# Performance work log

Measured on AMD Instinct MI355X. Metric: run time of the kernel, lower is better.

## Reference

```python
import jax, jax.numpy as jnp
import numpy as np

jax.config.update("jax_enable_x64", True)

NUM_OF_LSB_TO_IGNORE = 5
COMPARISON_NUM_BITS_IGNORED = 5
SCALE = 65536.0  # activations live on an integer-share-like scale so bit shifts matter

BLOCK_SIZES = np.array([[0, 1]] * 32 + [[2, 2]] * 48 + [[4, 4]] * 48)
# active (non-identity) block sizes and the channel indices they own
ACTIVE = [(tuple(int(v) for v in bs), np.where(np.all(BLOCK_SIZES == bs, axis=1))[0])
          for bs in np.unique(BLOCK_SIZES, axis=0) if 0 not in bs]


def setup_inputs() -> dict:
    key = jax.random.key(0)
    activation = jax.random.normal(key, (16, 128, 114, 114), dtype=jnp.float32) * SCALE
    return {"activation": activation}


def _block_sign(x, bh, bw):
    # x: [N, c, H, W]. Pad bottom/right to block multiples, space-to-depth,
    # integer floor-mean per block, LSB truncation via int16 wrap, sign >= 0.
    N, c, H, W = x.shape
    ph, pw = (-H) % bh, (-W) % bw
    xp = jnp.pad(x, ((0, 0), (0, 0), (0, ph), (0, pw)))
    xr = xp.reshape(N, c, (H + ph) // bh, bh, (W + pw) // bw, bw)
    s = xr.sum(axis=(3, 5)).astype(jnp.int64)          # block sums
    mean = s // (bh * bw)                               # integer floor mean
    q = ((mean >> NUM_OF_LSB_TO_IGNORE).astype(jnp.int16)
         .astype(jnp.int64)) << COMPARISON_NUM_BITS_IGNORED
    sign = q >= 0                                       # DReLU
    # broadcast block sign back to pixels, then unpad
    sign = jnp.repeat(jnp.repeat(sign, bh, axis=2), bw, axis=3)
    return sign[:, :, :H, :W]


def reference(activation):
    out = activation
    for (bh, bw), ch in ACTIVE:  # small fixed set of block-size groups
        cur = activation[:, ch]
        sign = _block_sign(cur, bh, bw)
        out = out.at[:, ch].set(cur * sign.astype(activation.dtype))
    return out
```

## Files before the change

### kernel.cpp

```cpp
#include <hip/hip_runtime.h>


typedef float v4 __attribute__((ext_vector_type(4)));

#define PLANE  12996
#define NBLK_A 6498
#define NU_B   43776
#define NBLK_B 10944
#define NU_C   22272
#define NBLK_C 5568

__global__ __launch_bounds__(256) void sbrelu_reg(const float* __restrict__ in,
                                                  float* __restrict__ out) {
    const int bid = blockIdx.x;
    const int tid = threadIdx.x;

    if (bid < NBLK_A) {
        int idx = bid * 256 + tid;
        int n = idx / 103968;
        int off = n * 415872 + (idx - n * 103968);
        ((v4*)out)[off] = ((const v4*)in)[off];
        return;
    }

    const int lane = tid & 63;
    const int wid  = tid >> 6;

    if (bid < NBLK_A + NBLK_B) {
        int u  = (bid - NBLK_A) * 4 + wid;
        int p  = u / 57;
        int rp = u - 57 * p;
        int n  = p / 48;
        int c  = 32 + (p - 48 * n);
        size_t base = (size_t)(n * 128 + c) * PLANE + 228 * rp;
        if (lane < 57) {
            const float2* i0 = (const float2*)(in + base) + lane;
            float2 a = i0[0];
            float2 b = i0[57];
            float s = ((a.x + a.y) + b.x) + b.y;
            float m = (s > -1.0f) ? 1.0f : 0.0f;
            float2* o0 = (float2*)(out + base) + lane;
            o0[0]  = make_float2(a.x * m, a.y * m);
            o0[57] = make_float2(b.x * m, b.y * m);
        }
        return;
    }

    int u  = (bid - NBLK_A - NBLK_B) * 4 + wid;
    int p  = u / 29;
    int br = u - 29 * p;
    int n  = p / 48;
    int c  = 80 + (p - 48 * n);
    size_t base = (size_t)(n * 128 + c) * PLANE + 456 * br;
    if (lane >= 29) return;
    const bool full = (lane != 28);
    const float2* q  = (const float2*)(in  + base) + 2 * lane;
    float2*       qo = (float2*)      (out + base) + 2 * lane;

    if (br != 28) {
        float2 a0 = q[0],  a1 = q[57],  a2 = q[114], a3 = q[171];
        float2 b0 = make_float2(0.f, 0.f), b1 = b0, b2 = b0, b3 = b0;
        if (full) { b0 = q[1]; b1 = q[58]; b2 = q[115]; b3 = q[172]; }
        float s = 0.0f;
        s += a0.x; s += a0.y; if (full) { s += b0.x; s += b0.y; }
        s += a1.x; s += a1.y; if (full) { s += b1.x; s += b1.y; }
        s += a2.x; s += a2.y; if (full) { s += b2.x; s += b2.y; }
        s += a3.x; s += a3.y; if (full) { s += b3.x; s += b3.y; }
        float m = (s > -1.0f) ? 1.0f : 0.0f;
        qo[0]   = make_float2(a0.x * m, a0.y * m);
        qo[57]  = make_float2(a1.x * m, a1.y * m);
        qo[114] = make_float2(a2.x * m, a2.y * m);
        qo[171] = make_float2(a3.x * m, a3.y * m);
        if (full) {
            qo[1]   = make_float2(b0.x * m, b0.y * m);
            qo[58]  = make_float2(b1.x * m, b1.y * m);
            qo[115] = make_float2(b2.x * m, b2.y * m);
            qo[172] = make_float2(b3.x * m, b3.y * m);
        }
    } else {
        float2 a0 = q[0], a1 = q[57];
        float2 b0 = make_float2(0.f, 0.f), b1 = b0;
        if (full) { b0 = q[1]; b1 = q[58]; }
        float s = 0.0f;
        s += a0.x; s += a0.y; if (full) { s += b0.x; s += b0.y; }
        s += a1.x; s += a1.y; if (full) { s += b1.x; s += b1.y; }
        float m = (s > -1.0f) ? 1.0f : 0.0f;
        qo[0]  = make_float2(a0.x * m, a0.y * m);
        qo[57] = make_float2(a1.x * m, a1.y * m);
        if (full) {
            qo[1]  = make_float2(b0.x * m, b0.y * m);
            qo[58] = make_float2(b1.x * m, b1.y * m);
        }
    }
}

extern "C" void kernel_launch(void* const* d_in, const int* in_sizes, int n_in,
                              void* d_out, int out_size, void* d_ws, size_t ws_size,
                              hipStream_t stream) {
    const float* in = (const float*)d_in[0];
    float* out = (float*)d_out;
    sbrelu_reg<<<NBLK_A + NBLK_B + NBLK_C, 256, 0, stream>>>(in, out);
}
```

Before: 187.2 us.

## Use persistent-style grid-stride blocks with batched loads for all three regions

Replaces the one-work-item-per-wave launch (about 23k blocks) with a fixed grid of 2048 blocks that loop over their region's work. The copy region issues four vector loads before its stores, and the 2x2 region processes four rows per iteration. The 4x4 region packs two block-rows per wave using both 32-lane halves, so fewer lanes sit idle. This aims to cut block launch overhead and raise memory-level parallelism per wave. The cost is a less even tail balance across CUs and more register pressure.

```diff
diff --git a/kernel.cpp b/kernel.cpp
--- a/kernel.cpp
+++ b/kernel.cpp
@@ -3,59 +3,56 @@
 
 typedef float v4 __attribute__((ext_vector_type(4)));
 
-#define PLANE  12996
-#define NBLK_A 6498
-#define NU_B   43776
-#define NBLK_B 10944
-#define NU_C   22272
-#define NBLK_C 5568
+#define PLANE     12996
+#define NA4       1663488
+#define A_PER_N   103968
+#define A_NSTRIDE 415872
+#define NB_A      512
+#define NB_B      768
+#define NB_C      768
+#define SW_B      3072
+#define SW_C      3072
+#define NU_B      43776
+#define NU_C      22272
+#define NPAIR_C   11136
 
-__global__ __launch_bounds__(256) void sbrelu_reg(const float* __restrict__ in,
-                                                  float* __restrict__ out) {
-    const int bid = blockIdx.x;
-    const int tid = threadIdx.x;
+__device__ __forceinline__ int amap(int idx) {
+    int n = idx / A_PER_N;
+    return n * A_NSTRIDE + (idx - n * A_PER_N);
+}
 
-    if (bid < NBLK_A) {
-        int idx = bid * 256 + tid;
-        int n = idx / 103968;
-        int off = n * 415872 + (idx - n * 103968);
-        ((v4*)out)[off] = ((const v4*)in)[off];
-        return;
-    }
+__device__ __forceinline__ size_t bbase(int u) {
+    int p  = u / 57;
+    int rp = u - 57 * p;
+    int n  = p / 48;
+    int c  = 32 + (p - 48 * n);
+    return (size_t)(n * 128 + c) * PLANE + 228 * rp;
+}
 
-    const int lane = tid & 63;
-    const int wid  = tid >> 6;
+__device__ __forceinline__ void bproc1(const float* __restrict__ in,
+                                       float* __restrict__ out,
+                                       int u, int lane) {
+    size_t b = bbase(u);
+    const float2* ip = (const float2*)(in + b) + lane;
+    float2 a = ip[0], c = ip[57];
+    float s = ((a.x + a.y) + c.x) + c.y;
+    float m = (s > -1.0f) ? 1.0f : 0.0f;
+    float2* op = (float2*)(out + b) + lane;
+    op[0]  = make_float2(a.x * m, a.y * m);
+    op[57] = make_float2(c.x * m, c.y * m);
+}
 
-    if (bid < NBLK_A + NBLK_B) {
-        int u  = (bid - NBLK_A) * 4 + wid;
-        int p  = u / 57;
-        int rp = u - 57 * p;
-        int n  = p / 48;
-        int c  = 32 + (p - 48 * n);
-        size_t base = (size_t)(n * 128 + c) * PLANE + 228 * rp;
-        if (lane < 57) {
-            const float2* i0 = (const float2*)(in + base) + lane;
-            float2 a = i0[0];
-            float2 b = i0[57];
-            float s = ((a.x + a.y) + b.x) + b.y;
-            float m = (s > -1.0f) ? 1.0f : 0.0f;
-            float2* o0 = (float2*)(out + base) + lane;
-            o0[0]  = make_float2(a.x * m, a.y * m);
-            o0[57] = make_float2(b.x * m, b.y * m);
-        }
-        return;
-    }
-
-    int u  = (bid - NBLK_A - NBLK_B) * 4 + wid;
+__device__ __forceinline__ void cproc1(const float* __restrict__ in,
+                                       float* __restrict__ out,
+                                       int u, int cb) {
     int p  = u / 29;
     int br = u - 29 * p;
     int n  = p / 48;
     int c  = 80 + (p - 48 * n);
     size_t base = (size_t)(n * 128 + c) * PLANE + 456 * br;
-    if (lane >= 29) return;
-    const bool full = (lane != 28);
-    const float2* q  = (const float2*)(in  + base) + 2 * lane;
-    float2*       qo = (float2*)      (out + base) + 2 * lane;
+    const bool full = (cb != 28);
+    const float2* q  = (const float2*)(in  + base) + 2 * cb;
+    float2*       qo = (float2*)      (out + base) + 2 * cb;
 
     if (br != 28) {
         float2 a0 = q[0],  a1 = q[57],  a2 = q[114], a3 = q[171];
@@ -94,10 +91,87 @@
     }
 }
 
+__global__ __launch_bounds__(256) void sbrelu_ps(const float* __restrict__ in,
+                                                 float* __restrict__ out) {
+    const int bid  = blockIdx.x;
+    const int tid  = threadIdx.x;
+    const int lane = tid & 63;
+    const int wid  = tid >> 6;
+
+    if (bid < NB_A) {
+        const v4* __restrict__ vin = (const v4*)in;
+        v4* __restrict__ vout = (v4*)out;
+        const int t = bid * 256 + tid;
+        const int S = NB_A * 256;
+        for (int base = 0; base < 12 * S; base += 4 * S) {
+            int o0 = amap(t + base);
+            int o1 = amap(t + base + S);
+            int o2 = amap(t + base + 2 * S);
+            int o3 = amap(t + base + 3 * S);
+            v4 x0 = vin[o0], x1 = vin[o1], x2 = vin[o2], x3 = vin[o3];
+            vout[o0] = x0; vout[o1] = x1; vout[o2] = x2; vout[o3] = x3;
+        }
+        int jt = t + 12 * S;
+        if (jt < NA4) { int o = amap(jt); vout[o] = vin[o]; }
+        return;
+    }
+
+    if (bid < NB_A + NB_B) {
+        if (lane >= 57) return;
+        const int wb = (bid - NB_A) * 4 + wid;
+        for (int k = 0; k < 12; k += 4) {
+            int u0 = wb + (k    ) * SW_B;
+            int u1 = wb + (k + 1) * SW_B;
+            int u2 = wb + (k + 2) * SW_B;
+            int u3 = wb + (k + 3) * SW_B;
+            size_t e0 = bbase(u0), e1 = bbase(u1), e2 = bbase(u2), e3 = bbase(u3);
+            const float2* p0 = (const float2*)(in + e0) + lane;
+            const float2* p1 = (const float2*)(in + e1) + lane;
+            const float2* p2 = (const float2*)(in + e2) + lane;
+            const float2* p3 = (const float2*)(in + e3) + lane;
+            float2 a0 = p0[0], c0 = p0[57];
+            float2 a1 = p1[0], c1 = p1[57];
+            float2 a2 = p2[0], c2 = p2[57];
+            float2 a3 = p3[0], c3 = p3[57];
+            float s0 = ((a0.x + a0.y) + c0.x) + c0.y;
+            float s1 = ((a1.x + a1.y) + c1.x) + c1.y;
+            float s2 = ((a2.x + a2.y) + c2.x) + c2.y;
+            float s3 = ((a3.x + a3.y) + c3.x) + c3.y;
+            float m0 = (s0 > -1.0f) ? 1.0f : 0.0f;
+            float m1 = (s1 > -1.0f) ? 1.0f : 0.0f;
+            float m2 = (s2 > -1.0f) ? 1.0f : 0.0f;
+            float m3 = (s3 > -1.0f) ? 1.0f : 0.0f;
+            float2* q0 = (float2*)(out + e0) + lane;
+            float2* q1 = (float2*)(out + e1) + lane;
+            float2* q2 = (float2*)(out + e2) + lane;
+            float2* q3 = (float2*)(out + e3) + lane;
+            q0[0] = make_float2(a0.x * m0, a0.y * m0); q0[57] = make_float2(c0.x * m0, c0.y * m0);
+            q1[0] = make_float2(a1.x * m1, a1.y * m1); q1[57] = make_float2(c1.x * m1, c1.y * m1);
+            q2[0] = make_float2(a2.x * m2, a2.y * m2); q2[57] = make_float2(c2.x * m2, c2.y * m2);
+            q3[0] = make_float2(a3.x * m3, a3.y * m3); q3[57] = make_float2(c3.x * m3, c3.y * m3);
+        }
+        bproc1(in, out, wb + 12 * SW_B, lane);
+        bproc1(in, out, wb + 13 * SW_B, lane);
+        int u = wb + 14 * SW_B;
+        if (u < NU_B) bproc1(in, out, u, lane);
+        return;
+    }
+
+    const int cb = lane & 31;
+    if (cb >= 29) return;
+    const int wc = (bid - NB_A - NB_B) * 4 + wid;
+    const int half = lane >> 5;
+    for (int k = 0; k < 4; ++k) {
+        int pr = k * SW_C + wc;
+        if (pr >= NPAIR_C) break;
+        cproc1(in, out, 2 * pr + half, cb);
+    }
+}
+
 extern "C" void kernel_launch(void* const* d_in, const int* in_sizes, int n_in,
                               void* d_out, int out_size, void* d_ws, size_t ws_size,
                               hipStream_t stream) {
     const float* in = (const float*)d_in[0];
     float* out = (float*)d_out;
-    sbrelu_reg<<<NBLK_A + NBLK_B + NBLK_C, 256, 0, stream>>>(in, out);
+    sbrelu_ps<<<NB_A + NB_B + NB_C, 256, 0, stream>>>(in, out);
 }
```

New measurement: 188.8 us. No clear change (+0.9%).

## Split into bulk copy plus sparse zeroing fixup kernels

Applied to the files above, without the earlier changes.

Replaces the single fused kernel with a bulk vectorized copy of the whole tensor, followed by two fixup kernels that re-read the blocked channels and write zeros only where the block sign is negative. The point is a simpler, fully coalesced copy and skipping stores for positive blocks. In exchange the blocked channels are read twice and written up to twice, and there are two extra kernel launches. It also relies on ordering between launches on the same stream.

```diff
diff --git a/kernel.cpp b/kernel.cpp
--- a/kernel.cpp
+++ b/kernel.cpp
@@ -4,49 +4,60 @@
 typedef float v4 __attribute__((ext_vector_type(4)));
 
 #define PLANE  12996
-#define NBLK_A 6498
+#define NTOT4  6653952
+#define CSTR   524288
 #define NU_B   43776
 #define NBLK_B 10944
 #define NU_C   22272
 #define NBLK_C 5568
 
-__global__ __launch_bounds__(256) void sbrelu_reg(const float* __restrict__ in,
-                                                  float* __restrict__ out) {
-    const int bid = blockIdx.x;
-    const int tid = threadIdx.x;
+__global__ __launch_bounds__(256) void copy_all(const float* __restrict__ in,
+                                                float* __restrict__ out) {
+    const v4* __restrict__ vin = (const v4*)in;
+    v4* __restrict__ vout = (v4*)out;
+    const int t = blockIdx.x * 256 + threadIdx.x;
+    for (int k = 0; k < 3; ++k) {
+        int b = k * 4 * CSTR + t;
+        v4 x0 = vin[b];
+        v4 x1 = vin[b + CSTR];
+        v4 x2 = vin[b + 2 * CSTR];
+        v4 x3 = vin[b + 3 * CSTR];
+        vout[b]            = x0;
+        vout[b + CSTR]     = x1;
+        vout[b + 2 * CSTR] = x2;
+        vout[b + 3 * CSTR] = x3;
+    }
+    int r = 12 * CSTR + t;
+    if (r < NTOT4) vout[r] = vin[r];
+}
 
-    if (bid < NBLK_A) {
-        int idx = bid * 256 + tid;
-        int n = idx / 103968;
-        int off = n * 415872 + (idx - n * 103968);
-        ((v4*)out)[off] = ((const v4*)in)[off];
-        return;
+__global__ __launch_bounds__(256) void fixup_b(const float* __restrict__ in,
+                                               float* __restrict__ out) {
+    const int lane = threadIdx.x & 63;
+    int u  = blockIdx.x * 4 + (threadIdx.x >> 6);
+    int p  = u / 57;
+    int rp = u - 57 * p;
+    int n  = p / 48;
+    int c  = 32 + (p - 48 * n);
+    size_t base = (size_t)(n * 128 + c) * PLANE + 228 * rp;
+    if (lane < 57) {
+        const float2* i0 = (const float2*)(in + base) + lane;
+        float2 a = i0[0];
+        float2 b = i0[57];
+        float s = ((a.x + a.y) + b.x) + b.y;
+        if (!(s > -1.0f)) {
+            float2* o0 = (float2*)(out + base) + lane;
+            float2 z = make_float2(0.f, 0.f);
+            o0[0]  = z;
+            o0[57] = z;
+        }
     }
+}
 
-    const int lane = tid & 63;
-    const int wid  = tid >> 6;
-
-    if (bid < NBLK_A + NBLK_B) {
-        int u  = (bid - NBLK_A) * 4 + wid;
-        int p  = u / 57;
-        int rp = u - 57 * p;
-        int n  = p / 48;
-        int c  = 32 + (p - 48 * n);
-        size_t base = (size_t)(n * 128 + c) * PLANE + 228 * rp;
-        if (lane < 57) {
-            const float2* i0 = (const float2*)(in + base) + lane;
-            float2 a = i0[0];
-            float2 b = i0[57];
-            float s = ((a.x + a.y) + b.x) + b.y;
-            float m = (s > -1.0f) ? 1.0f : 0.0f;
-            float2* o0 = (float2*)(out + base) + lane;
-            o0[0]  = make_float2(a.x * m, a.y * m);
-            o0[57] = make_float2(b.x * m, b.y * m);
-        }
-        return;
-    }
-
-    int u  = (bid - NBLK_A - NBLK_B) * 4 + wid;
+__global__ __launch_bounds__(256) void fixup_c(const float* __restrict__ in,
+                                               float* __restrict__ out) {
+    const int lane = threadIdx.x & 63;
+    int u  = blockIdx.x * 4 + (threadIdx.x >> 6);
     int p  = u / 29;
     int br = u - 29 * p;
     int n  = p / 48;
@@ -56,40 +67,31 @@
     const bool full = (lane != 28);
     const float2* q  = (const float2*)(in  + base) + 2 * lane;
     float2*       qo = (float2*)      (out + base) + 2 * lane;
+    const float2 z = make_float2(0.f, 0.f);
 
     if (br != 28) {
         float2 a0 = q[0],  a1 = q[57],  a2 = q[114], a3 = q[171];
-        float2 b0 = make_float2(0.f, 0.f), b1 = b0, b2 = b0, b3 = b0;
+        float2 b0 = z, b1 = z, b2 = z, b3 = z;
         if (full) { b0 = q[1]; b1 = q[58]; b2 = q[115]; b3 = q[172]; }
         float s = 0.0f;
         s += a0.x; s += a0.y; if (full) { s += b0.x; s += b0.y; }
         s += a1.x; s += a1.y; if (full) { s += b1.x; s += b1.y; }
         s += a2.x; s += a2.y; if (full) { s += b2.x; s += b2.y; }
         s += a3.x; s += a3.y; if (full) { s += b3.x; s += b3.y; }
-        float m = (s > -1.0f) ? 1.0f : 0.0f;
-        qo[0]   = make_float2(a0.x * m, a0.y * m);
-        qo[57]  = make_float2(a1.x * m, a1.y * m);
-        qo[114] = make_float2(a2.x * m, a2.y * m);
-        qo[171] = make_float2(a3.x * m, a3.y * m);
-        if (full) {
-            qo[1]   = make_float2(b0.x * m, b0.y * m);
-            qo[58]  = make_float2(b1.x * m, b1.y * m);
-            qo[115] = make_float2(b2.x * m, b2.y * m);
-            qo[172] = make_float2(b3.x * m, b3.y * m);
+        if (!(s > -1.0f)) {
+            qo[0] = z; qo[57] = z; qo[114] = z; qo[171] = z;
+            if (full) { qo[1] = z; qo[58] = z; qo[115] = z; qo[172] = z; }
         }
     } else {
         float2 a0 = q[0], a1 = q[57];
-        float2 b0 = make_float2(0.f, 0.f), b1 = b0;
+        float2 b0 = z, b1 = z;
         if (full) { b0 = q[1]; b1 = q[58]; }
         float s = 0.0f;
         s += a0.x; s += a0.y; if (full) { s += b0.x; s += b0.y; }
         s += a1.x; s += a1.y; if (full) { s += b1.x; s += b1.y; }
-        float m = (s > -1.0f) ? 1.0f : 0.0f;
-        qo[0]  = make_float2(a0.x * m, a0.y * m);
-        qo[57] = make_float2(a1.x * m, a1.y * m);
-        if (full) {
-            qo[1]  = make_float2(b0.x * m, b0.y * m);
-            qo[58] = make_float2(b1.x * m, b1.y * m);
+        if (!(s > -1.0f)) {
+            qo[0] = z; qo[57] = z;
+            if (full) { qo[1] = z; qo[58] = z; }
         }
     }
 }
@@ -99,5 +101,7 @@
                               hipStream_t stream) {
     const float* in = (const float*)d_in[0];
     float* out = (float*)d_out;
-    sbrelu_reg<<<NBLK_A + NBLK_B + NBLK_C, 256, 0, stream>>>(in, out);
+    copy_all<<<2048, 256, 0, stream>>>(in, out);
+    fixup_b<<<NBLK_B, 256, 0, stream>>>(in, out);
+    fixup_c<<<NBLK_C, 256, 0, stream>>>(in, out);
 }
```

New measurement: 224.6 us. 1.2x slower.
